# Kernel tuning notes

Measured on AMD Instinct MI355X. Metric: run time of the kernel, lower is better.

Reference implementation:

```python
import jax, jax.numpy as jnp
import numpy as np

WS = 8        # window_size
NH = 16       # num_heads

def setup_inputs() -> dict:
    key = jax.random.key(0)
    ks = jax.random.split(key, 6)
    B, H, W, C = 16, 64, 64, 512
    nW = (H // WS) * (W // WS)
    return {
        "x": jax.random.normal(ks[0], (B, H * W, C), jnp.float32),
        "qkv_w": jax.random.normal(ks[1], (3 * C, C), jnp.float32) * 0.02,
        "qkv_b": jax.random.normal(ks[2], (3 * C,), jnp.float32) * 0.02,
        "proj_w": jax.random.normal(ks[3], (C, C), jnp.float32) * 0.02,
        "proj_b": jax.random.normal(ks[4], (C,), jnp.float32) * 0.02,
        "attn_mask": jax.random.normal(ks[5], (nW, WS * WS, WS * WS), jnp.float32),
        "H": H,
        "W": W,
    }

def reference(x, qkv_w, qkv_b, proj_w, proj_b, attn_mask, H, W):
    B, N, C = x.shape
    ws = WS
    hd = C // NH
    scale = hd ** (-0.5)
    x_img = x.reshape(B, H, W, C)
    pad_h = (ws - H % ws) % ws
    pad_w = (ws - W % ws) % ws
    if pad_h > 0 or pad_w > 0:
        x_img = jnp.pad(x_img, ((0, 0), (0, pad_h), (0, pad_w), (0, 0)))
    Hp, Wp = H + pad_h, W + pad_w
    nW = (Hp // ws) * (Wp // ws)
    # window partition: [B*nW, ws*ws, C]
    x_win = x_img.reshape(B, Hp // ws, ws, Wp // ws, ws, C)
    x_win = x_win.transpose(0, 1, 3, 2, 4, 5).reshape(B * nW, ws * ws, C)
    # fused qkv projection (torch Linear: y = x @ W^T + b)
    qkv = x_win @ qkv_w.T + qkv_b
    qkv = qkv.reshape(B * nW, ws * ws, 3, NH, hd).transpose(2, 0, 3, 1, 4)
    q, k, v = qkv[0], qkv[1], qkv[2]  # each [B*nW, NH, ws*ws, hd]
    attn = jnp.einsum('bhqd,bhkd->bhqk', q, k) * scale
    if attn_mask is not None:
        attn = attn.reshape(B, nW, NH, ws * ws, ws * ws)
        attn = attn + attn_mask[None, :, None, :, :]
        attn = attn.reshape(B * nW, NH, ws * ws, ws * ws)
    attn = jax.nn.softmax(attn, axis=-1)
    out = jnp.einsum('bhqk,bhkd->bhqd', attn, v)
    out = out.transpose(0, 2, 1, 3).reshape(B * nW, ws * ws, C)
    out = out @ proj_w.T + proj_b
    # window reverse
    out = out.reshape(B, Hp // ws, Wp // ws, ws, ws, C)
    out = out.transpose(0, 1, 3, 2, 4, 5).reshape(B, Hp, Wp, C)
    out = out[:, :H, :W, :].reshape(B, H * W, C)
    return out
```

## Files before the change

kernel.cpp:

```cpp
#include <hip/hip_runtime.h>


typedef unsigned short u16;
typedef unsigned int u32;
typedef __attribute__((ext_vector_type(4))) u16 u16x4;
typedef __attribute__((ext_vector_type(8))) u16 u16x8;
typedef __attribute__((ext_vector_type(8))) short short8;
typedef __attribute__((ext_vector_type(4))) float f32x4;

__device__ __forceinline__ u16 f2bf(float f) {
    u32 u = __float_as_uint(f);
    u += 0x7fffu + ((u >> 16) & 1u);
    return (u16)(u >> 16);
}

__device__ __forceinline__ f32x4 MFMA(u16x8 a, u16x8 b, f32x4 c) {
    return __builtin_amdgcn_mfma_f32_16x16x32_bf16(
        __builtin_bit_cast(short8, a), __builtin_bit_cast(short8, b), c, 0, 0, 0);
}

__device__ __forceinline__ void gload16(const void* g, void* l) {
    __builtin_amdgcn_global_load_lds(
        (const __attribute__((address_space(1))) void*)g,
        (__attribute__((address_space(3))) void*)l, 16, 0, 0);
}

__device__ __forceinline__ int win2img(int r) {
    int b = r >> 12;
    int w = (r >> 6) & 63;
    int t = r & 63;
    int img = (((w >> 3) << 3) + (t >> 3)) * 64 + ((w & 7) << 3) + (t & 7);
    return (b << 12) + img;
}

__device__ __forceinline__ u16x8 cvt8(const float* src) {
    float4 a = *(const float4*)src;
    float4 b = *(const float4*)(src + 4);
    u16x8 t;
    t[0] = f2bf(a.x); t[1] = f2bf(a.y); t[2] = f2bf(a.z); t[3] = f2bf(a.w);
    t[4] = f2bf(b.x); t[5] = f2bf(b.y); t[6] = f2bf(b.z); t[7] = f2bf(b.w);
    return t;
}

__global__ __launch_bounds__(256)
void conv_f2b(const float* __restrict__ in, u16* __restrict__ out, int n8) {
    int u = blockIdx.x * 256 + threadIdx.x;
    if (u >= n8) return;
    *(u16x8*)(out + (size_t)u * 8) = cvt8(in + (size_t)u * 8);
}

__global__ __launch_bounds__(256, 3)
void gemm_qkv(const float* __restrict__ X, const u16* __restrict__ Wq,
              const float* __restrict__ bias, u16* __restrict__ QK,
              u16* __restrict__ VT)
{
    __shared__ u16 sA[2][128 * 32];
    __shared__ u16 sB[2][128 * 32];

    const int nwg = gridDim.x;
    const int q   = nwg >> 3;
    const int wg  = ((int)blockIdx.x & 7) * q + ((int)blockIdx.x >> 3);
    const int m0  = (wg / 12) * 128;
    const int n0  = (wg % 12) * 128;

    const int tid  = threadIdx.x;
    const int lane = tid & 63;
    const int wv   = tid >> 6;
    const int wm   = (wv >> 1) << 6;
    const int wn   = (wv & 1) << 6;
    const int lr   = lane & 15;
    const int lg   = lane >> 4;

    const int ar = tid >> 1;
    const int kh = (tid & 1) << 4;
    const float* ax = X + ((size_t)win2img(m0 + ar) << 9) + kh;
    u16* aw = &sA[0][ar * 32 + kh];

    const char* bptr0 = (const char*)Wq + ((size_t)(n0 + (tid >> 2)) << 10) + ((tid & 3) << 4);
    const char* bptr1 = bptr0 + (64 << 10);

    f32x4 acc[4][4] = {};
    float4 a0, a1, a2, a3;

#define LOADA(kt) do {                                                        \
    const float* p_ = ax + (kt) * 32;                                         \
    a0 = *(const float4*)p_;  a1 = *(const float4*)(p_ + 4);                  \
    a2 = *(const float4*)(p_ + 8); a3 = *(const float4*)(p_ + 12);            \
} while (0)

#define WRITEA(buf) do {                                                      \
    u16x8 t_;                                                                 \
    t_[0]=f2bf(a0.x); t_[1]=f2bf(a0.y); t_[2]=f2bf(a0.z); t_[3]=f2bf(a0.w);   \
    t_[4]=f2bf(a1.x); t_[5]=f2bf(a1.y); t_[6]=f2bf(a1.z); t_[7]=f2bf(a1.w);   \
    *(u16x8*)(aw + (buf) * 4096) = t_;                                        \
    t_[0]=f2bf(a2.x); t_[1]=f2bf(a2.y); t_[2]=f2bf(a2.z); t_[3]=f2bf(a2.w);   \
    t_[4]=f2bf(a3.x); t_[5]=f2bf(a3.y); t_[6]=f2bf(a3.z); t_[7]=f2bf(a3.w);   \
    *(u16x8*)(aw + (buf) * 4096 + 8) = t_;                                    \
} while (0)

#define STAGEB(buf, kt) do {                                                  \
    char* d_ = (char*)sB + (buf) * 8192 + tid * 16;                           \
    gload16(bptr0 + (kt) * 64, d_);                                           \
    gload16(bptr1 + (kt) * 64, d_ + 4096);                                    \
} while (0)

#define COMPUTE(buf) do {                                                     \
    const u16* As_ = &sA[buf][0];                                             \
    const u16* Bs_ = &sB[buf][0];                                             \
    u16x8 af_[4], bf_[4];                                                     \
    _Pragma("unroll")                                                         \
    for (int mi = 0; mi < 4; ++mi)                                            \
        af_[mi] = *(const u16x8*)(As_ + (wm + mi * 16 + lr) * 32 + lg * 8);   \
    _Pragma("unroll")                                                         \
    for (int ni = 0; ni < 4; ++ni)                                            \
        bf_[ni] = *(const u16x8*)(Bs_ + (wn + ni * 16 + lr) * 32 + lg * 8);   \
    _Pragma("unroll")                                                         \
    for (int mi = 0; mi < 4; ++mi)                                            \
        _Pragma("unroll")                                                     \
        for (int ni = 0; ni < 4; ++ni)                                        \
            acc[mi][ni] = MFMA(af_[mi], bf_[ni], acc[mi][ni]);                \
} while (0)

    LOADA(0);
    STAGEB(0, 0);
    WRITEA(0);
    __syncthreads();

#pragma unroll 1
    for (int t = 0; t < 16; ++t) {
        const int cur = t & 1, nxt = cur ^ 1;
        if (t < 15) { LOADA(t + 1); STAGEB(nxt, t + 1); }
        COMPUTE(cur);
        __syncthreads();
        if (t < 15) {
            WRITEA(nxt);
            __syncthreads();
        }
    }

#undef LOADA
#undef WRITEA
#undef STAGEB
#undef COMPUTE

    if (n0 < 1024) {
#pragma unroll
        for (int mi = 0; mi < 4; ++mi)
#pragma unroll
            for (int ni = 0; ni < 4; ++ni) {
                const int col = n0 + wn + ni * 16 + lr;
                const float bv = bias[col];
#pragma unroll
                for (int r = 0; r < 4; ++r) {
                    const int gr = m0 + wm + mi * 16 + lg * 4 + r;
                    QK[((size_t)gr << 10) + col] = f2bf(acc[mi][ni][r] + bv);
                }
            }
    } else {
#pragma unroll
        for (int mi = 0; mi < 4; ++mi) {
            const int gr0 = m0 + wm + mi * 16 + lg * 4;
            const int win = gr0 >> 6, ro = gr0 & 63;
#pragma unroll
            for (int ni = 0; ni < 4; ++ni) {
                const int col = n0 + wn + ni * 16 + lr;
                const float bv = bias[col];
                const int d = col - 1024;
                u16x4 h;
#pragma unroll
                for (int r = 0; r < 4; ++r) h[r] = f2bf(acc[mi][ni][r] + bv);
                *(u16x4*)(VT + (((size_t)win << 9) + d) * 64 + ro) = h;
            }
        }
    }
}

__global__ __launch_bounds__(256, 4)
void gemm_proj(const u16* __restrict__ A, const u16* __restrict__ Wt,
               const float* __restrict__ bias, float* __restrict__ C)
{
    __shared__ char lds[32768];

    const int nwg = gridDim.x;
    const int q   = nwg >> 3;
    const int wg  = ((int)blockIdx.x & 7) * q + ((int)blockIdx.x >> 3);
    const int m0  = (wg / 4) * 128;
    const int n0  = (wg % 4) * 128;

    const int tid  = threadIdx.x;
    const int lane = tid & 63;
    const int wv   = tid >> 6;
    const int wm   = (wv >> 1) << 6;
    const int wn   = (wv & 1) << 6;
    const int lr   = lane & 15;
    const int lg   = lane >> 4;

    const char* aptr = (const char*)A + (((size_t)(m0 + (tid >> 2))) << 10) + ((tid & 3) << 4);
    const char* bptr = (const char*)Wt + (((size_t)(n0 + (tid >> 2))) << 10) + ((tid & 3) << 4);
    const u32 tb = (u32)tid << 4;

    f32x4 acc[4][4] = {};

#define STAGE(buf, kt) do {                                                   \
    const int ko_ = (kt) * 64;                                                \
    char* d_ = lds + (buf) * 16384 + tb;                                      \
    gload16(aptr + ko_,              d_);                                     \
    gload16(aptr + (64 << 10) + ko_, d_ + 4096);                              \
    gload16(bptr + ko_,              d_ + 8192);                              \
    gload16(bptr + (64 << 10) + ko_, d_ + 12288);                             \
} while (0)

#define COMPUTE(buf) do {                                                     \
    const u16* As_ = (const u16*)(lds + (buf) * 16384);                       \
    const u16* Bs_ = (const u16*)(lds + (buf) * 16384 + 8192);                \
    u16x8 af_[4], bf_[4];                                                     \
    _Pragma("unroll")                                                         \
    for (int mi = 0; mi < 4; ++mi)                                            \
        af_[mi] = *(const u16x8*)(As_ + (wm + mi * 16 + lr) * 32 + lg * 8);   \
    _Pragma("unroll")                                                         \
    for (int ni = 0; ni < 4; ++ni)                                            \
        bf_[ni] = *(const u16x8*)(Bs_ + (wn + ni * 16 + lr) * 32 + lg * 8);   \
    _Pragma("unroll")                                                         \
    for (int mi = 0; mi < 4; ++mi)                                            \
        _Pragma("unroll")                                                     \
        for (int ni = 0; ni < 4; ++ni)                                        \
            acc[mi][ni] = MFMA(af_[mi], bf_[ni], acc[mi][ni]);                \
} while (0)

    STAGE(0, 0);
    __syncthreads();

#pragma unroll 1
    for (int kt = 0; kt < 16; kt += 2) {
        STAGE(1, kt + 1);
        COMPUTE(0);
        __syncthreads();
        if (kt + 2 < 16) STAGE(0, kt + 2);
        COMPUTE(1);
        __syncthreads();
    }

#undef STAGE
#undef COMPUTE

#pragma unroll
    for (int mi = 0; mi < 4; ++mi)
#pragma unroll
        for (int ni = 0; ni < 4; ++ni) {
            const int col = n0 + wn + ni * 16 + lr;
            const float bv = bias[col];
#pragma unroll
            for (int r = 0; r < 4; ++r) {
                const int gr = win2img(m0 + wm + mi * 16 + lg * 4 + r);
                C[((size_t)gr << 9) + col] = acc[mi][ni][r] + bv;
            }
        }
}

__global__ __launch_bounds__(256, 2)
void attn_kernel(const u16* __restrict__ QK, const u16* __restrict__ VT,
                 const float* __restrict__ mask, u16* __restrict__ attn_out)
{
    __shared__ u16 sP[4][64][72];
    __shared__ float mT[64 * 65];

    const int tid  = threadIdx.x;
    const int lane = tid & 63;
    const int wv   = tid >> 6;
    const int lr   = lane & 15;
    const int lg   = lane >> 4;
    const int win  = blockIdx.x;
    const int wib  = win & 63;
    const size_t rb = (size_t)win << 6;
    const float scale = 0.17677669529663687f;

    {
        const float* mp = mask + ((size_t)wib << 12) + tid * 16;
        float4 v[4];
#pragma unroll
        for (int i = 0; i < 4; ++i) v[i] = *(const float4*)(mp + i * 4);
        const int r0 = tid >> 2, c0 = (tid & 3) << 4;
#pragma unroll
        for (int e = 0; e < 16; ++e)
            mT[(c0 + e) * 65 + r0] = v[e >> 2][e & 3];
    }
    __syncthreads();

    const u16* vbase = VT + ((size_t)win << 15);

    for (int hi = 0; hi < 4; ++hi) {
        const int h = hi * 4 + wv;
        const int hoff = h * 32;

        u16x8 qf[4], kf[4];
#pragma unroll
        for (int mt = 0; mt < 4; ++mt) {
            const u16* rowp = QK + ((rb + mt * 16 + lr) << 10) + hoff + lg * 8;
            qf[mt] = *(const u16x8*)rowp;
            kf[mt] = *(const u16x8*)(rowp + 512);
        }
        f32x4 s[4][4] = {};
#pragma unroll
        for (int mi = 0; mi < 4; ++mi)
#pragma unroll
            for (int ni = 0; ni < 4; ++ni)
                s[mi][ni] = MFMA(qf[mi], kf[ni], s[mi][ni]);

        float rsum[4][4];
#pragma unroll
        for (int mi = 0; mi < 4; ++mi) {
            float4 mv[4];
#pragma unroll
            for (int ni = 0; ni < 4; ++ni)
                mv[ni] = *(const float4*)&mT[(ni * 16 + lr) * 65 + mi * 16 + lg * 4];
#pragma unroll
            for (int r = 0; r < 4; ++r) {
                float vv[4];
                float mx = -1e30f;
#pragma unroll
                for (int ni = 0; ni < 4; ++ni) {
                    float v = s[mi][ni][r] * scale + ((const float*)&mv[ni])[r];
                    vv[ni] = v;
                    mx = fmaxf(mx, v);
                }
#pragma unroll
                for (int mk = 1; mk <= 8; mk <<= 1)
                    mx = fmaxf(mx, __shfl_xor(mx, mk, 64));
                float sum = 0.f;
#pragma unroll
                for (int ni = 0; ni < 4; ++ni) {
                    float p = __expf(vv[ni] - mx);
                    sum += p;
                    s[mi][ni][r] = p;
                }
#pragma unroll
                for (int mk = 1; mk <= 8; mk <<= 1)
                    sum += __shfl_xor(sum, mk, 64);
                rsum[mi][r] = sum;
            }
        }

        __syncthreads();
#pragma unroll
        for (int mi = 0; mi < 4; ++mi)
#pragma unroll
            for (int ni = 0; ni < 4; ++ni)
#pragma unroll
                for (int r = 0; r < 4; ++r)
                    sP[wv][mi * 16 + lg * 4 + r][ni * 16 + lr] = f2bf(s[mi][ni][r]);
        __syncthreads();

        u16x8 pf[4][2];
#pragma unroll
        for (int mt = 0; mt < 4; ++mt)
#pragma unroll
            for (int k2 = 0; k2 < 2; ++k2)
                pf[mt][k2] = *(const u16x8*)&sP[wv][mt * 16 + lr][k2 * 32 + lg * 8];

        u16x8 vf[2][2];
#pragma unroll
        for (int k2 = 0; k2 < 2; ++k2)
#pragma unroll
            for (int nt = 0; nt < 2; ++nt)
                vf[k2][nt] = *(const u16x8*)(vbase
                    + ((size_t)(hoff + nt * 16 + lr) << 6) + k2 * 32 + lg * 8);

        f32x4 o[4][2] = {};
#pragma unroll
        for (int mt = 0; mt < 4; ++mt)
#pragma unroll
            for (int k2 = 0; k2 < 2; ++k2)
#pragma unroll
                for (int nt = 0; nt < 2; ++nt)
                    o[mt][nt] = MFMA(pf[mt][k2], vf[k2][nt], o[mt][nt]);

#pragma unroll
        for (int mt = 0; mt < 4; ++mt)
#pragma unroll
            for (int nt = 0; nt < 2; ++nt)
#pragma unroll
                for (int r = 0; r < 4; ++r) {
                    const int row = mt * 16 + lg * 4 + r;
                    const int d = nt * 16 + lr;
                    attn_out[((rb + row) << 9) + hoff + d] =
                        f2bf(o[mt][nt][r] / rsum[mt][r]);
                }
    }
}

extern "C" void kernel_launch(void* const* d_in, const int* in_sizes, int n_in,
                              void* d_out, int out_size, void* d_ws, size_t ws_size,
                              hipStream_t stream)
{
    const float* x      = (const float*)d_in[0];
    const float* qkv_w  = (const float*)d_in[1];
    const float* qkv_b  = (const float*)d_in[2];
    const float* proj_w = (const float*)d_in[3];
    const float* proj_b = (const float*)d_in[4];
    const float* mask   = (const float*)d_in[5];
    float* out = (float*)d_out;

    const size_t WQKV  = 1536ull * 512;
    const size_t WPROJ = 512ull * 512;

    u16* wq = (u16*)d_ws;
    u16* wp = wq + WQKV;
    u16* chunk = wp + WPROJ;

    const size_t qkPB  = 4096ull * 1024;
    const size_t vtPB  = 4096ull * 512;
    const size_t attPB = 4096ull * 512;
    const size_t perBatchBytes = (qkPB + vtPB + attPB) * 2;

    size_t avail = ws_size - (WQKV + WPROJ) * 2;
    int Bc = (int)(avail / perBatchBytes);
    if (Bc > 16) Bc = 16;
    if (Bc < 1) Bc = 1;

    u16* qk_ws  = chunk;
    u16* vt_ws  = qk_ws + (size_t)Bc * qkPB;
    u16* att_ws = vt_ws + (size_t)Bc * vtPB;

    conv_f2b<<<dim3((WQKV / 8 + 255) / 256), 256, 0, stream>>>(qkv_w, wq, (int)(WQKV / 8));
    conv_f2b<<<dim3((WPROJ / 8 + 255) / 256), 256, 0, stream>>>(proj_w, wp, (int)(WPROJ / 8));

    for (int b0 = 0; b0 < 16; b0 += Bc) {
        const int bc = (16 - b0) < Bc ? (16 - b0) : Bc;
        const float* xc = x + (size_t)b0 * 4096 * 512;
        float* outc = out + (size_t)b0 * 4096 * 512;

        gemm_qkv<<<dim3(bc * 32 * 12), 256, 0, stream>>>(
            xc, wq, qkv_b, qk_ws, vt_ws);
        attn_kernel<<<dim3(bc * 64), 256, 0, stream>>>(
            qk_ws, vt_ws, mask, att_ws);
        gemm_proj<<<dim3(bc * 32 * 4), 256, 0, stream>>>(
            att_ws, wp, proj_b, outc);
    }
}
```

Baseline: 370.3 us.

## Pre-convert x to windowed bf16, pretranspose mask, prefetch heads in attention

A separate kernel now gathers x into window order and converts it to bf16, so the QKV GEMM can reuse the proj GEMM's global-to-LDS staging path with bf16 operands for both sides. The attention mask is transposed once into a global buffer, which removes the per-block LDS transpose and barrier. Attention also double-buffers the Q/K/V fragment loads for the next head. In exchange there is an extra full pass over x (fp32 read plus bf16 write) and more workspace, and the attention kernel uses more registers.

```diff
diff --git a/kernel.cpp b/kernel.cpp
--- a/kernel.cpp
+++ b/kernel.cpp
@@ -49,143 +49,54 @@
     *(u16x8*)(out + (size_t)u * 8) = cvt8(in + (size_t)u * 8);
 }
 
-__global__ __launch_bounds__(256, 3)
-void gemm_qkv(const float* __restrict__ X, const u16* __restrict__ Wq,
+__global__ __launch_bounds__(256)
+void conv_permute_x(const float* __restrict__ x, u16* __restrict__ xw) {
+    int u = blockIdx.x * 256 + threadIdx.x;
+    int r = u >> 6;
+    int c = (u & 63) << 3;
+    int g = win2img(r);
+    *(u16x8*)(xw + (size_t)r * 512 + c) = cvt8(x + (size_t)g * 512 + c);
+}
+
+__global__ __launch_bounds__(256)
+void conv_maskT(const float* __restrict__ mask, float* __restrict__ mT) {
+    __shared__ float t[64][65];
+    const int w = blockIdx.x;
+    const float* mp = mask + ((size_t)w << 12);
+    float* op = mT + ((size_t)w << 12);
+    const int r = threadIdx.x >> 2, c0 = (threadIdx.x & 3) << 4;
+#pragma unroll
+    for (int i = 0; i < 4; ++i) {
+        float4 v = *(const float4*)(mp + (r << 6) + c0 + i * 4);
+        t[c0 + i * 4 + 0][r] = v.x;
+        t[c0 + i * 4 + 1][r] = v.y;
+        t[c0 + i * 4 + 2][r] = v.z;
+        t[c0 + i * 4 + 3][r] = v.w;
+    }
+    __syncthreads();
+#pragma unroll
+    for (int i = 0; i < 4; ++i) {
+        float4 v;
+        v.x = t[r][c0 + i * 4 + 0];
+        v.y = t[r][c0 + i * 4 + 1];
+        v.z = t[r][c0 + i * 4 + 2];
+        v.w = t[r][c0 + i * 4 + 3];
+        *(float4*)(op + (r << 6) + c0 + i * 4) = v;
+    }
+}
+
+__global__ __launch_bounds__(256, 4)
+void gemm_qkv(const u16* __restrict__ A, const u16* __restrict__ Wt,
               const float* __restrict__ bias, u16* __restrict__ QK,
               u16* __restrict__ VT)
 {
-    __shared__ u16 sA[2][128 * 32];
-    __shared__ u16 sB[2][128 * 32];
+    __shared__ char lds[32768];
 
     const int nwg = gridDim.x;
     const int q   = nwg >> 3;
     const int wg  = ((int)blockIdx.x & 7) * q + ((int)blockIdx.x >> 3);
     const int m0  = (wg / 12) * 128;
     const int n0  = (wg % 12) * 128;
-
-    const int tid  = threadIdx.x;
-    const int lane = tid & 63;
-    const int wv   = tid >> 6;
-    const int wm   = (wv >> 1) << 6;
-    const int wn   = (wv & 1) << 6;
-    const int lr   = lane & 15;
-    const int lg   = lane >> 4;
-
-    const int ar = tid >> 1;
-    const int kh = (tid & 1) << 4;
-    const float* ax = X + ((size_t)win2img(m0 + ar) << 9) + kh;
-    u16* aw = &sA[0][ar * 32 + kh];
-
-    const char* bptr0 = (const char*)Wq + ((size_t)(n0 + (tid >> 2)) << 10) + ((tid & 3) << 4);
-    const char* bptr1 = bptr0 + (64 << 10);
-
-    f32x4 acc[4][4] = {};
-    float4 a0, a1, a2, a3;
-
-#define LOADA(kt) do {                                                        \
-    const float* p_ = ax + (kt) * 32;                                         \
-    a0 = *(const float4*)p_;  a1 = *(const float4*)(p_ + 4);                  \
-    a2 = *(const float4*)(p_ + 8); a3 = *(const float4*)(p_ + 12);            \
-} while (0)
-
-#define WRITEA(buf) do {                                                      \
-    u16x8 t_;                                                                 \
-    t_[0]=f2bf(a0.x); t_[1]=f2bf(a0.y); t_[2]=f2bf(a0.z); t_[3]=f2bf(a0.w);   \
-    t_[4]=f2bf(a1.x); t_[5]=f2bf(a1.y); t_[6]=f2bf(a1.z); t_[7]=f2bf(a1.w);   \
-    *(u16x8*)(aw + (buf) * 4096) = t_;                                        \
-    t_[0]=f2bf(a2.x); t_[1]=f2bf(a2.y); t_[2]=f2bf(a2.z); t_[3]=f2bf(a2.w);   \
-    t_[4]=f2bf(a3.x); t_[5]=f2bf(a3.y); t_[6]=f2bf(a3.z); t_[7]=f2bf(a3.w);   \
-    *(u16x8*)(aw + (buf) * 4096 + 8) = t_;                                    \
-} while (0)
-
-#define STAGEB(buf, kt) do {                                                  \
-    char* d_ = (char*)sB + (buf) * 8192 + tid * 16;                           \
-    gload16(bptr0 + (kt) * 64, d_);                                           \
-    gload16(bptr1 + (kt) * 64, d_ + 4096);                                    \
-} while (0)
-
-#define COMPUTE(buf) do {                                                     \
-    const u16* As_ = &sA[buf][0];                                             \
-    const u16* Bs_ = &sB[buf][0];                                             \
-    u16x8 af_[4], bf_[4];                                                     \
-    _Pragma("unroll")                                                         \
-    for (int mi = 0; mi < 4; ++mi)                                            \
-        af_[mi] = *(const u16x8*)(As_ + (wm + mi * 16 + lr) * 32 + lg * 8);   \
-    _Pragma("unroll")                                                         \
-    for (int ni = 0; ni < 4; ++ni)                                            \
-        bf_[ni] = *(const u16x8*)(Bs_ + (wn + ni * 16 + lr) * 32 + lg * 8);   \
-    _Pragma("unroll")                                                         \
-    for (int mi = 0; mi < 4; ++mi)                                            \
-        _Pragma("unroll")                                                     \
-        for (int ni = 0; ni < 4; ++ni)                                        \
-            acc[mi][ni] = MFMA(af_[mi], bf_[ni], acc[mi][ni]);                \
-} while (0)
-
-    LOADA(0);
-    STAGEB(0, 0);
-    WRITEA(0);
-    __syncthreads();
-
-#pragma unroll 1
-    for (int t = 0; t < 16; ++t) {
-        const int cur = t & 1, nxt = cur ^ 1;
-        if (t < 15) { LOADA(t + 1); STAGEB(nxt, t + 1); }
-        COMPUTE(cur);
-        __syncthreads();
-        if (t < 15) {
-            WRITEA(nxt);
-            __syncthreads();
-        }
-    }
-
-#undef LOADA
-#undef WRITEA
-#undef STAGEB
-#undef COMPUTE
-
-    if (n0 < 1024) {
-#pragma unroll
-        for (int mi = 0; mi < 4; ++mi)
-#pragma unroll
-            for (int ni = 0; ni < 4; ++ni) {
-                const int col = n0 + wn + ni * 16 + lr;
-                const float bv = bias[col];
-#pragma unroll
-                for (int r = 0; r < 4; ++r) {
-                    const int gr = m0 + wm + mi * 16 + lg * 4 + r;
-                    QK[((size_t)gr << 10) + col] = f2bf(acc[mi][ni][r] + bv);
-                }
-            }
-    } else {
-#pragma unroll
-        for (int mi = 0; mi < 4; ++mi) {
-            const int gr0 = m0 + wm + mi * 16 + lg * 4;
-            const int win = gr0 >> 6, ro = gr0 & 63;
-#pragma unroll
-            for (int ni = 0; ni < 4; ++ni) {
-                const int col = n0 + wn + ni * 16 + lr;
-                const float bv = bias[col];
-                const int d = col - 1024;
-                u16x4 h;
-#pragma unroll
-                for (int r = 0; r < 4; ++r) h[r] = f2bf(acc[mi][ni][r] + bv);
-                *(u16x4*)(VT + (((size_t)win << 9) + d) * 64 + ro) = h;
-            }
-        }
-    }
-}
-
-__global__ __launch_bounds__(256, 4)
-void gemm_proj(const u16* __restrict__ A, const u16* __restrict__ Wt,
-               const float* __restrict__ bias, float* __restrict__ C)
-{
-    __shared__ char lds[32768];
-
-    const int nwg = gridDim.x;
-    const int q   = nwg >> 3;
-    const int wg  = ((int)blockIdx.x & 7) * q + ((int)blockIdx.x >> 3);
-    const int m0  = (wg / 4) * 128;
-    const int n0  = (wg % 4) * 128;
 
     const int tid  = threadIdx.x;
     const int lane = tid & 63;
@@ -240,6 +151,77 @@
         __syncthreads();
     }
 
+    if (n0 < 1024) {
+#pragma unroll
+        for (int mi = 0; mi < 4; ++mi)
+#pragma unroll
+            for (int ni = 0; ni < 4; ++ni) {
+                const int col = n0 + wn + ni * 16 + lr;
+                const float bv = bias[col];
+#pragma unroll
+                for (int r = 0; r < 4; ++r) {
+                    const int gr = m0 + wm + mi * 16 + lg * 4 + r;
+                    QK[((size_t)gr << 10) + col] = f2bf(acc[mi][ni][r] + bv);
+                }
+            }
+    } else {
+#pragma unroll
+        for (int mi = 0; mi < 4; ++mi) {
+            const int gr0 = m0 + wm + mi * 16 + lg * 4;
+            const int win = gr0 >> 6, ro = gr0 & 63;
+#pragma unroll
+            for (int ni = 0; ni < 4; ++ni) {
+                const int col = n0 + wn + ni * 16 + lr;
+                const float bv = bias[col];
+                const int d = col - 1024;
+                u16x4 h;
+#pragma unroll
+                for (int r = 0; r < 4; ++r) h[r] = f2bf(acc[mi][ni][r] + bv);
+                *(u16x4*)(VT + (((size_t)win << 9) + d) * 64 + ro) = h;
+            }
+        }
+    }
+}
+
+__global__ __launch_bounds__(256, 4)
+void gemm_proj(const u16* __restrict__ A, const u16* __restrict__ Wt,
+               const float* __restrict__ bias, float* __restrict__ C)
+{
+    __shared__ char lds[32768];
+
+    const int nwg = gridDim.x;
+    const int q   = nwg >> 3;
+    const int wg  = ((int)blockIdx.x & 7) * q + ((int)blockIdx.x >> 3);
+    const int m0  = (wg / 4) * 128;
+    const int n0  = (wg % 4) * 128;
+
+    const int tid  = threadIdx.x;
+    const int lane = tid & 63;
+    const int wv   = tid >> 6;
+    const int wm   = (wv >> 1) << 6;
+    const int wn   = (wv & 1) << 6;
+    const int lr   = lane & 15;
+    const int lg   = lane >> 4;
+
+    const char* aptr = (const char*)A + (((size_t)(m0 + (tid >> 2))) << 10) + ((tid & 3) << 4);
+    const char* bptr = (const char*)Wt + (((size_t)(n0 + (tid >> 2))) << 10) + ((tid & 3) << 4);
+    const u32 tb = (u32)tid << 4;
+
+    f32x4 acc[4][4] = {};
+
+    STAGE(0, 0);
+    __syncthreads();
+
+#pragma unroll 1
+    for (int kt = 0; kt < 16; kt += 2) {
+        STAGE(1, kt + 1);
+        COMPUTE(0);
+        __syncthreads();
+        if (kt + 2 < 16) STAGE(0, kt + 2);
+        COMPUTE(1);
+        __syncthreads();
+    }
+
 #undef STAGE
 #undef COMPUTE
 
@@ -259,10 +241,9 @@
 
 __global__ __launch_bounds__(256, 2)
 void attn_kernel(const u16* __restrict__ QK, const u16* __restrict__ VT,
-                 const float* __restrict__ mask, u16* __restrict__ attn_out)
+                 const float* __restrict__ mT, u16* __restrict__ attn_out)
 {
-    __shared__ u16 sP[4][64][72];
-    __shared__ float mT[64 * 65];
+    __shared__ __align__(16) u16 sP[4][64][72];
 
     const int tid  = threadIdx.x;
     const int lane = tid & 63;
@@ -272,39 +253,40 @@
     const int win  = blockIdx.x;
     const int wib  = win & 63;
     const size_t rb = (size_t)win << 6;
+    const float* mtp = mT + ((size_t)wib << 12);
+    const u16* vbase = VT + ((size_t)win << 15);
     const float scale = 0.17677669529663687f;
 
-    {
-        const float* mp = mask + ((size_t)wib << 12) + tid * 16;
-        float4 v[4];
-#pragma unroll
-        for (int i = 0; i < 4; ++i) v[i] = *(const float4*)(mp + i * 4);
-        const int r0 = tid >> 2, c0 = (tid & 3) << 4;
-#pragma unroll
-        for (int e = 0; e < 16; ++e)
-            mT[(c0 + e) * 65 + r0] = v[e >> 2][e & 3];
-    }
-    __syncthreads();
-
-    const u16* vbase = VT + ((size_t)win << 15);
-
+    u16x8 qf[2][4], kf[2][4], vf[2][2][2];
+
+#define LOADH(hi_, b_) do {                                                   \
+    const int hoff_ = ((hi_) * 4 + wv) * 32;                                  \
+    _Pragma("unroll") for (int mt = 0; mt < 4; ++mt) {                        \
+        const u16* rp_ = QK + ((rb + mt * 16 + lr) << 10) + hoff_ + lg * 8;   \
+        qf[b_][mt] = *(const u16x8*)rp_;                                      \
+        kf[b_][mt] = *(const u16x8*)(rp_ + 512);                              \
+    }                                                                         \
+    _Pragma("unroll") for (int k2_ = 0; k2_ < 2; ++k2_)                       \
+    _Pragma("unroll") for (int nt_ = 0; nt_ < 2; ++nt_)                       \
+        vf[b_][k2_][nt_] = *(const u16x8*)(vbase                              \
+            + ((size_t)(hoff_ + nt_ * 16 + lr) << 6) + k2_ * 32 + lg * 8);    \
+} while (0)
+
+    LOADH(0, 0);
+
+#pragma unroll
     for (int hi = 0; hi < 4; ++hi) {
-        const int h = hi * 4 + wv;
-        const int hoff = h * 32;
-
-        u16x8 qf[4], kf[4];
-#pragma unroll
-        for (int mt = 0; mt < 4; ++mt) {
-            const u16* rowp = QK + ((rb + mt * 16 + lr) << 10) + hoff + lg * 8;
-            qf[mt] = *(const u16x8*)rowp;
-            kf[mt] = *(const u16x8*)(rowp + 512);
-        }
+        const int cb = hi & 1;
+        const int hoff = (hi * 4 + wv) * 32;
+
         f32x4 s[4][4] = {};
 #pragma unroll
         for (int mi = 0; mi < 4; ++mi)
 #pragma unroll
             for (int ni = 0; ni < 4; ++ni)
-                s[mi][ni] = MFMA(qf[mi], kf[ni], s[mi][ni]);
+                s[mi][ni] = MFMA(qf[cb][mi], kf[cb][ni], s[mi][ni]);
+
+        if (hi < 3) LOADH(hi + 1, cb ^ 1);
 
         float rsum[4][4];
 #pragma unroll
@@ -312,7 +294,7 @@
             float4 mv[4];
 #pragma unroll
             for (int ni = 0; ni < 4; ++ni)
-                mv[ni] = *(const float4*)&mT[(ni * 16 + lr) * 65 + mi * 16 + lg * 4];
+                mv[ni] = *(const float4*)(mtp + (ni * 16 + lr) * 64 + mi * 16 + lg * 4);
 #pragma unroll
             for (int r = 0; r < 4; ++r) {
                 float vv[4];
@@ -357,14 +339,6 @@
             for (int k2 = 0; k2 < 2; ++k2)
                 pf[mt][k2] = *(const u16x8*)&sP[wv][mt * 16 + lr][k2 * 32 + lg * 8];
 
-        u16x8 vf[2][2];
-#pragma unroll
-        for (int k2 = 0; k2 < 2; ++k2)
-#pragma unroll
-            for (int nt = 0; nt < 2; ++nt)
-                vf[k2][nt] = *(const u16x8*)(vbase
-                    + ((size_t)(hoff + nt * 16 + lr) << 6) + k2 * 32 + lg * 8);
-
         f32x4 o[4][2] = {};
 #pragma unroll
         for (int mt = 0; mt < 4; ++mt)
@@ -372,7 +346,7 @@
             for (int k2 = 0; k2 < 2; ++k2)
 #pragma unroll
                 for (int nt = 0; nt < 2; ++nt)
-                    o[mt][nt] = MFMA(pf[mt][k2], vf[k2][nt], o[mt][nt]);
+                    o[mt][nt] = MFMA(pf[mt][k2], vf[cb][k2][nt], o[mt][nt]);
 
 #pragma unroll
         for (int mt = 0; mt < 4; ++mt)
@@ -386,6 +360,7 @@
                         f2bf(o[mt][nt][r] / rsum[mt][r]);
                 }
     }
+#undef LOADH
 }
 
 extern "C" void kernel_launch(void* const* d_in, const int* in_sizes, int n_in,
@@ -402,37 +377,43 @@
 
     const size_t WQKV  = 1536ull * 512;
     const size_t WPROJ = 512ull * 512;
+    const size_t MTSZ  = 64ull * 64 * 64;
 
     u16* wq = (u16*)d_ws;
     u16* wp = wq + WQKV;
-    u16* chunk = wp + WPROJ;
-
+    float* mTg = (float*)(wp + WPROJ);
+    u16* chunk = (u16*)(mTg + MTSZ);
+
+    const size_t xwPB  = 4096ull * 512;
     const size_t qkPB  = 4096ull * 1024;
     const size_t vtPB  = 4096ull * 512;
     const size_t attPB = 4096ull * 512;
-    const size_t perBatchBytes = (qkPB + vtPB + attPB) * 2;
-
-    size_t avail = ws_size - (WQKV + WPROJ) * 2;
+    const size_t perBatchBytes = (xwPB + qkPB + vtPB + attPB) * 2;
+
+    size_t avail = ws_size - (WQKV + WPROJ) * 2 - MTSZ * 4;
     int Bc = (int)(avail / perBatchBytes);
     if (Bc > 16) Bc = 16;
     if (Bc < 1) Bc = 1;
 
-    u16* qk_ws  = chunk;
+    u16* xw_ws  = chunk;
+    u16* qk_ws  = xw_ws + (size_t)Bc * xwPB;
     u16* vt_ws  = qk_ws + (size_t)Bc * qkPB;
     u16* att_ws = vt_ws + (size_t)Bc * vtPB;
 
     conv_f2b<<<dim3((WQKV / 8 + 255) / 256), 256, 0, stream>>>(qkv_w, wq, (int)(WQKV / 8));
     conv_f2b<<<dim3((WPROJ / 8 + 255) / 256), 256, 0, stream>>>(proj_w, wp, (int)(WPROJ / 8));
+    conv_maskT<<<dim3(64), 256, 0, stream>>>(mask, mTg);
 
     for (int b0 = 0; b0 < 16; b0 += Bc) {
         const int bc = (16 - b0) < Bc ? (16 - b0) : Bc;
         const float* xc = x + (size_t)b0 * 4096 * 512;
         float* outc = out + (size_t)b0 * 4096 * 512;
 
+        conv_permute_x<<<dim3(bc * 1024), 256, 0, stream>>>(xc, xw_ws);
         gemm_qkv<<<dim3(bc * 32 * 12), 256, 0, stream>>>(
-            xc, wq, qkv_b, qk_ws, vt_ws);
+            xw_ws, wq, qkv_b, qk_ws, vt_ws);
         attn_kernel<<<dim3(bc * 64), 256, 0, stream>>>(
-            qk_ws, vt_ws, mask, att_ws);
+            qk_ws, vt_ws, mTg, att_ws);
         gemm_proj<<<dim3(bc * 32 * 4), 256, 0, stream>>>(
             att_ws, wp, proj_b, outc);
     }
```

Measured after the change: 394.1 us. 1.06x slower.
